# Optimization experiments

Measured on AMD Instinct MI355X. Metric: run time of the kernel, lower is better.

## Reference

```python
import jax, jax.numpy as jnp
import numpy as np

DIM = 64  # QK head dim, matches init kwarg 'dim'

def setup_inputs() -> dict:
    key = jax.random.key(0)
    kq, kk, kv = jax.random.split(key, 3)
    B, L, C, D, H = 2, 2048, 16, DIM, 64
    query = jax.random.normal(kq, (B, L, C, D), dtype=jnp.float32)
    k_ = jax.random.normal(kk, (B, L, C, D), dtype=jnp.float32)
    value = jax.random.normal(kv, (B, L, C, H), dtype=jnp.float32)
    return {"query": query, "key": k_, "value": value}

def reference(query, key, value):
    scaler = 1.0 / jnp.sqrt(jnp.float32(DIM))
    # score: [b, c, l, m]
    score = jnp.einsum('blcd,bmcd->bclm', query, key) * scaler
    # mask=False, dropout=0 -> identity
    attn = jax.nn.softmax(score, axis=3)
    # out: [b, l, c, h]
    out = jnp.einsum('bmch,bclm->blch', value, attn)
    return out
```

## Files before the change

kernel.cpp:

```cpp
#include <hip/hip_runtime.h>
#include <hip/hip_bf16.h>
#include <stdint.h>

#define B_ 2
#define L_ 2048
#define C_ 16
#define D_ 64
#define H_ 64
#define QBLK 128
#define KVBLK 64
#define NTILES 32
#define NTHREADS 256
#define NHEADS 32
#define TILE_ELEMS 4096
#define TENSOR_ELEMS (NHEADS * NTILES * TILE_ELEMS)

typedef __attribute__((ext_vector_type(8))) short bf16x8;
typedef __attribute__((ext_vector_type(16))) float f32x16;
typedef __attribute__((ext_vector_type(8))) unsigned short u16x8;

__device__ inline unsigned short f2bf(float f) {
  union { float f; unsigned int u; } v; v.f = f;
  unsigned int u = v.u;
  unsigned int r = (u + 0x7FFFu + ((u >> 16) & 1u)) >> 16;
  return (unsigned short)r;
}

__device__ inline float fast_exp2(float x) {
#if __has_builtin(__builtin_amdgcn_exp2f)
  return __builtin_amdgcn_exp2f(x);
#else
  return exp2f(x);
#endif
}

__device__ inline unsigned cvt_pk_bf16(float lo, float hi) {
  unsigned r;
  asm("v_cvt_pk_bf16_f32 %0, %1, %2" : "=v"(r) : "v"(lo), "v"(hi));
  return r;
}

__device__ inline void pl32swap(unsigned &x, unsigned &y) {
#if __has_builtin(__builtin_amdgcn_permlane32_swap)
  auto r = __builtin_amdgcn_permlane32_swap(x, y, false, false);
  x = r[0]; y = r[1];
#else
  asm("v_permlane32_swap_b32 %0, %1" : "+v"(x), "+&v"(y));
#endif
}

__device__ inline float xsum32(float v) {
  unsigned x = __float_as_uint(v), y = x;
  pl32swap(x, y);
  return __uint_as_float(x) + __uint_as_float(y);
}

__global__ __launch_bounds__(256) void prepack_kernel(
    const float* __restrict__ Kg, const float* __restrict__ Vg,
    unsigned short* __restrict__ Kb, unsigned short* __restrict__ Vb) {
  int idx = blockIdx.x * 256 + threadIdx.x;
  if (idx < 524288) {
    int i = idx;
    int lane = i & 63, frag = (i >> 6) & 7, t = (i >> 9) & 31, head = i >> 14;
    int b = head >> 4, c = head & 15;
    int ks = frag >> 1, half = frag & 1;
    int row = half * 32 + (lane & 31);
    int kb = ks * 16 + (lane >> 5) * 8;
    const float* src = Kg + ((size_t)(b * L_ + t * 64 + row) * C_ + c) * D_ + kb;
    float4 a0 = ((const float4*)src)[0];
    float4 a1 = ((const float4*)src)[1];
    u16x8 pk;
    pk[0] = f2bf(a0.x); pk[1] = f2bf(a0.y); pk[2] = f2bf(a0.z); pk[3] = f2bf(a0.w);
    pk[4] = f2bf(a1.x); pk[5] = f2bf(a1.y); pk[6] = f2bf(a1.z); pk[7] = f2bf(a1.w);
    size_t dst = ((((size_t)(head * 32 + t)) * 8 + frag) * 64 + lane) * 8;
    *(u16x8*)&Kb[dst] = pk;
  } else {
    int i = idx - 524288;
    int lane = i & 63, frag = (i >> 6) & 7, t = (i >> 9) & 31, head = i >> 14;
    int b = head >> 4, c = head & 15;
    int m = frag >> 1, half = frag & 1;
    int h = half * 32 + (lane & 31);
    int kv0 = m * 16 + (lane >> 5) * 8;
    const float* src = Vg + ((size_t)(b * L_ + t * 64 + kv0) * C_ + c) * H_ + h;
    u16x8 pv;
#pragma unroll
    for (int j = 0; j < 8; ++j) pv[j] = f2bf(src[(size_t)j * C_ * H_]);
    size_t dst = ((((size_t)(head * 32 + t)) * 8 + frag) * 64 + lane) * 8;
    *(u16x8*)&Vb[dst] = pv;
  }
}

#define SM_PV(S0, S1, O0, O1, L)                                                  \
  {                                                                               \
    float rst[4];                                                                 \
    bf16x8 pf[4];                                                                 \
    _Pragma("unroll")                                                             \
    for (int tq = 0; tq < 4; ++tq) {                                              \
      const int be = ((2 * tq) & 3) * 4;                                          \
      const int bo = ((2 * tq + 1) & 3) * 4;                                      \
      float p0[4], p1[4];                                                         \
      _Pragma("unroll")                                                           \
      for (int r = 0; r < 4; ++r) {                                               \
        float se = (tq < 2) ? S0[be + r] : S1[be + r];                            \
        float so_ = (tq < 2) ? S0[bo + r] : S1[bo + r];                           \
        p0[r] = fast_exp2(se);                                                    \
        p1[r] = fast_exp2(so_);                                                   \
      }                                                                           \
      rst[tq] = ((p0[0] + p0[1]) + (p0[2] + p0[3])) +                             \
                ((p1[0] + p1[1]) + (p1[2] + p1[3]));                              \
      unsigned x0 = cvt_pk_bf16(p0[0], p0[1]);                                    \
      unsigned x1 = cvt_pk_bf16(p0[2], p0[3]);                                    \
      unsigned y0 = cvt_pk_bf16(p1[0], p1[1]);                                    \
      unsigned y1 = cvt_pk_bf16(p1[2], p1[3]);                                    \
      pl32swap(x0, y0);                                                           \
      pl32swap(x1, y1);                                                           \
      union { unsigned wd[4]; bf16x8 v; } pk_;                                    \
      pk_.wd[0] = x0; pk_.wd[1] = x1; pk_.wd[2] = y0; pk_.wd[3] = y1;             \
      pf[tq] = pk_.v;                                                             \
    }                                                                             \
    L += (rst[0] + rst[1]) + (rst[2] + rst[3]);                                   \
    __builtin_amdgcn_s_setprio(1);                                                \
    O0 = __builtin_amdgcn_mfma_f32_32x32x16_bf16(vc00, pf[0], O0, 0, 0, 0);       \
    O1 = __builtin_amdgcn_mfma_f32_32x32x16_bf16(vc01, pf[0], O1, 0, 0, 0);       \
    O0 = __builtin_amdgcn_mfma_f32_32x32x16_bf16(vc02, pf[1], O0, 0, 0, 0);       \
    O1 = __builtin_amdgcn_mfma_f32_32x32x16_bf16(vc03, pf[1], O1, 0, 0, 0);       \
    O0 = __builtin_amdgcn_mfma_f32_32x32x16_bf16(vc10, pf[2], O0, 0, 0, 0);       \
    O1 = __builtin_amdgcn_mfma_f32_32x32x16_bf16(vc11, pf[2], O1, 0, 0, 0);       \
    O0 = __builtin_amdgcn_mfma_f32_32x32x16_bf16(vc12, pf[3], O0, 0, 0, 0);       \
    O1 = __builtin_amdgcn_mfma_f32_32x32x16_bf16(vc13, pf[3], O1, 0, 0, 0);       \
    __builtin_amdgcn_s_setprio(0);                                                \
  }

__global__ __launch_bounds__(NTHREADS, 2) void attn_fwd_kernel(
    const float* __restrict__ Qg,
    const unsigned short* __restrict__ Kb,
    const unsigned short* __restrict__ Vb,
    float* __restrict__ Og) {
  __shared__ float Osh[2 * 64 * 68];
  __shared__ float lsh[2 * 2 * 64];

  const int tid  = threadIdx.x;
  const int lane = tid & 63;
  const int w    = tid >> 6;
  const int qw   = w >> 1;
  const int g    = w & 1;
  const int ql   = lane & 31;
  const int u    = lane >> 5;

  const int bid   = blockIdx.x;
  const int swz   = (bid & 7) * 64 + (bid >> 3);
  const int head  = swz >> 4;
  const int qtile = swz & 15;
  const int b     = head >> 4;
  const int c     = head & 15;
  const int q0    = qtile * QBLK + qw * 64;

  const unsigned short* KbL = Kb + (size_t)head * NTILES * TILE_ELEMS + lane * 8;
  const unsigned short* VbL = Vb + (size_t)head * NTILES * TILE_ELEMS + lane * 8;

  const float sc2 = 0.125f * 1.44269504088896340736f;
  bf16x8 qf0[4], qf1[4];
#pragma unroll
  for (int h = 0; h < 2; ++h) {
    const int qr = q0 + h * 32 + ql;
    const float* qrow = Qg + ((size_t)(b * L_ + qr) * C_ + c) * D_;
#pragma unroll
    for (int ks = 0; ks < 4; ++ks) {
      float4 a0 = *(const float4*)(qrow + ks * 16 + u * 8);
      float4 a1 = *(const float4*)(qrow + ks * 16 + u * 8 + 4);
      bf16x8 q8;
      q8[0] = (short)f2bf(a0.x * sc2); q8[1] = (short)f2bf(a0.y * sc2);
      q8[2] = (short)f2bf(a0.z * sc2); q8[3] = (short)f2bf(a0.w * sc2);
      q8[4] = (short)f2bf(a1.x * sc2); q8[5] = (short)f2bf(a1.y * sc2);
      q8[6] = (short)f2bf(a1.z * sc2); q8[7] = (short)f2bf(a1.w * sc2);
      if (h == 0) qf0[ks] = q8; else qf1[ks] = q8;
    }
  }

  f32x16 o00, o01, o10, o11;
#pragma unroll
  for (int i = 0; i < 16; ++i) { o00[i] = 0.f; o01[i] = 0.f; o10[i] = 0.f; o11[i] = 0.f; }
  float l0 = 0.f, l1 = 0.f;

  bf16x8 kc00, kc01, kc02, kc03;
  {
    const unsigned short* K0 = KbL + (size_t)g * TILE_ELEMS;
    kc00 = *(const bf16x8*)(K0);
    kc01 = *(const bf16x8*)(K0 + 512);
    kc02 = *(const bf16x8*)(K0 + 1024);
    kc03 = *(const bf16x8*)(K0 + 1536);
  }

  for (int tt = 0; tt < NTILES / 2; ++tt) {
    const int t = g + 2 * tt;
    const int tn = (tt + 1 < NTILES / 2) ? t + 2 : t;
    const unsigned short* Kt = KbL + (size_t)t * TILE_ELEMS;
    const unsigned short* Vt = VbL + (size_t)t * TILE_ELEMS;

    bf16x8 kc10 = *(const bf16x8*)(Kt + 2048);
    bf16x8 kc11 = *(const bf16x8*)(Kt + 2560);
    bf16x8 kc12 = *(const bf16x8*)(Kt + 3072);
    bf16x8 kc13 = *(const bf16x8*)(Kt + 3584);
    bf16x8 vc00 = *(const bf16x8*)(Vt);
    bf16x8 vc01 = *(const bf16x8*)(Vt + 512);
    bf16x8 vc02 = *(const bf16x8*)(Vt + 1024);
    bf16x8 vc03 = *(const bf16x8*)(Vt + 1536);
    bf16x8 vc10 = *(const bf16x8*)(Vt + 2048);
    bf16x8 vc11 = *(const bf16x8*)(Vt + 2560);
    bf16x8 vc12 = *(const bf16x8*)(Vt + 3072);
    bf16x8 vc13 = *(const bf16x8*)(Vt + 3584);

    f32x16 s00, s01, s10, s11;
#pragma unroll
    for (int i = 0; i < 16; ++i) { s00[i] = 0.f; s01[i] = 0.f; s10[i] = 0.f; s11[i] = 0.f; }
    __builtin_amdgcn_s_setprio(1);
    s00 = __builtin_amdgcn_mfma_f32_32x32x16_bf16(kc00, qf0[0], s00, 0, 0, 0);
    s01 = __builtin_amdgcn_mfma_f32_32x32x16_bf16(kc01, qf0[0], s01, 0, 0, 0);
    s10 = __builtin_amdgcn_mfma_f32_32x32x16_bf16(kc00, qf1[0], s10, 0, 0, 0);
    s11 = __builtin_amdgcn_mfma_f32_32x32x16_bf16(kc01, qf1[0], s11, 0, 0, 0);
    s00 = __builtin_amdgcn_mfma_f32_32x32x16_bf16(kc02, qf0[1], s00, 0, 0, 0);
    s01 = __builtin_amdgcn_mfma_f32_32x32x16_bf16(kc03, qf0[1], s01, 0, 0, 0);
    s10 = __builtin_amdgcn_mfma_f32_32x32x16_bf16(kc02, qf1[1], s10, 0, 0, 0);
    s11 = __builtin_amdgcn_mfma_f32_32x32x16_bf16(kc03, qf1[1], s11, 0, 0, 0);
    s00 = __builtin_amdgcn_mfma_f32_32x32x16_bf16(kc10, qf0[2], s00, 0, 0, 0);
    s01 = __builtin_amdgcn_mfma_f32_32x32x16_bf16(kc11, qf0[2], s01, 0, 0, 0);
    s10 = __builtin_amdgcn_mfma_f32_32x32x16_bf16(kc10, qf1[2], s10, 0, 0, 0);
    s11 = __builtin_amdgcn_mfma_f32_32x32x16_bf16(kc11, qf1[2], s11, 0, 0, 0);
    s00 = __builtin_amdgcn_mfma_f32_32x32x16_bf16(kc12, qf0[3], s00, 0, 0, 0);
    s01 = __builtin_amdgcn_mfma_f32_32x32x16_bf16(kc13, qf0[3], s01, 0, 0, 0);
    s10 = __builtin_amdgcn_mfma_f32_32x32x16_bf16(kc12, qf1[3], s10, 0, 0, 0);
    s11 = __builtin_amdgcn_mfma_f32_32x32x16_bf16(kc13, qf1[3], s11, 0, 0, 0);
    __builtin_amdgcn_s_setprio(0);

    {
      const unsigned short* Kn = KbL + (size_t)tn * TILE_ELEMS;
      kc00 = *(const bf16x8*)(Kn);
      kc01 = *(const bf16x8*)(Kn + 512);
      kc02 = *(const bf16x8*)(Kn + 1024);
      kc03 = *(const bf16x8*)(Kn + 1536);
    }

    SM_PV(s00, s01, o00, o01, l0);
    SM_PV(s10, s11, o10, o11, l1);
  }

  float la0 = xsum32(l0), la1 = xsum32(l1);
  float* Ow = &Osh[(qw * 64 + lane) * 68];
  if (g == 1) {
#pragma unroll
    for (int rg = 0; rg < 4; ++rg) {
      *(float4*)(Ow + rg * 4)      = (float4){o00[rg*4+0], o00[rg*4+1], o00[rg*4+2], o00[rg*4+3]};
      *(float4*)(Ow + 16 + rg * 4) = (float4){o01[rg*4+0], o01[rg*4+1], o01[rg*4+2], o01[rg*4+3]};
      *(float4*)(Ow + 32 + rg * 4) = (float4){o10[rg*4+0], o10[rg*4+1], o10[rg*4+2], o10[rg*4+3]};
      *(float4*)(Ow + 48 + rg * 4) = (float4){o11[rg*4+0], o11[rg*4+1], o11[rg*4+2], o11[rg*4+3]};
    }
    lsh[(qw * 2 + 0) * 64 + lane] = la0;
    lsh[(qw * 2 + 1) * 64 + lane] = la1;
  }
  __syncthreads();
  if (g == 0) {
    const float inv0 = 1.0f / (la0 + lsh[(qw * 2 + 0) * 64 + lane]);
    const float inv1 = 1.0f / (la1 + lsh[(qw * 2 + 1) * 64 + lane]);
    const int qr0 = q0 + ql;
    const int qr1 = q0 + 32 + ql;
    float* orow0 = Og + ((size_t)(b * L_ + qr0) * C_ + c) * H_;
    float* orow1 = Og + ((size_t)(b * L_ + qr1) * C_ + c) * H_;
#pragma unroll
    for (int rg = 0; rg < 4; ++rg) {
      float4 a0 = *(const float4*)(Ow + rg * 4);
      float4 a1 = *(const float4*)(Ow + 16 + rg * 4);
      float4 a2 = *(const float4*)(Ow + 32 + rg * 4);
      float4 a3 = *(const float4*)(Ow + 48 + rg * 4);
      float4 v0, v1, v2, v3;
      v0.x = (o00[rg*4+0] + a0.x) * inv0; v0.y = (o00[rg*4+1] + a0.y) * inv0;
      v0.z = (o00[rg*4+2] + a0.z) * inv0; v0.w = (o00[rg*4+3] + a0.w) * inv0;
      v1.x = (o01[rg*4+0] + a1.x) * inv0; v1.y = (o01[rg*4+1] + a1.y) * inv0;
      v1.z = (o01[rg*4+2] + a1.z) * inv0; v1.w = (o01[rg*4+3] + a1.w) * inv0;
      v2.x = (o10[rg*4+0] + a2.x) * inv1; v2.y = (o10[rg*4+1] + a2.y) * inv1;
      v2.z = (o10[rg*4+2] + a2.z) * inv1; v2.w = (o10[rg*4+3] + a2.w) * inv1;
      v3.x = (o11[rg*4+0] + a3.x) * inv1; v3.y = (o11[rg*4+1] + a3.y) * inv1;
      v3.z = (o11[rg*4+2] + a3.z) * inv1; v3.w = (o11[rg*4+3] + a3.w) * inv1;
      *(float4*)(orow0 + 8 * rg + 4 * u) = v0;
      *(float4*)(orow0 + 32 + 8 * rg + 4 * u) = v1;
      *(float4*)(orow1 + 8 * rg + 4 * u) = v2;
      *(float4*)(orow1 + 32 + 8 * rg + 4 * u) = v3;
    }
  }
}

extern "C" void kernel_launch(void* const* d_in, const int* in_sizes, int n_in,
                              void* d_out, int out_size, void* d_ws, size_t ws_size,
                              hipStream_t stream) {
  const float* Qg = (const float*)d_in[0];
  const float* Kg = (const float*)d_in[1];
  const float* Vg = (const float*)d_in[2];
  float* Og = (float*)d_out;

  unsigned short* Kb = (unsigned short*)d_ws;
  unsigned short* Vb = Kb + (size_t)TENSOR_ELEMS;

  prepack_kernel<<<4096, 256, 0, stream>>>(Kg, Vg, Kb, Vb);

  dim3 grid(NHEADS * (L_ / QBLK));
  dim3 block(NTHREADS);
  attn_fwd_kernel<<<grid, block, 0, stream>>>(Qg, Kb, Vb, Og);
}
```

Before: 64.89 us.

## Rotate K/V fragment registers and merge PV MFMAs across both query halves

Reuses two rotating sets of four bf16x8 register fragments (ka*, kb*) for K and V operands, interleaving their loads between the QK and PV MFMA groups, instead of holding twelve fragments live at once. The softmax for both query halves now runs first, and the PV MFMAs for both halves are then issued together and share each V fragment. The aim is lower register pressure and loads that are software-pipelined behind MFMA work. The trade-off is that more loads now sit directly on the dependency chain between MFMA groups, which can expose load latency.

```diff
diff --git a/kernel.cpp b/kernel.cpp
--- a/kernel.cpp
+++ b/kernel.cpp
@@ -90,10 +90,9 @@
   }
 }
 
-#define SM_PV(S0, S1, O0, O1, L)                                                  \
+#define SM(S0, S1, PF, L)                                                         \
   {                                                                               \
     float rst[4];                                                                 \
-    bf16x8 pf[4];                                                                 \
     _Pragma("unroll")                                                             \
     for (int tq = 0; tq < 4; ++tq) {                                              \
       const int be = ((2 * tq) & 3) * 4;                                          \
@@ -116,19 +115,9 @@
       pl32swap(x1, y1);                                                           \
       union { unsigned wd[4]; bf16x8 v; } pk_;                                    \
       pk_.wd[0] = x0; pk_.wd[1] = x1; pk_.wd[2] = y0; pk_.wd[3] = y1;             \
-      pf[tq] = pk_.v;                                                             \
+      PF[tq] = pk_.v;                                                             \
     }                                                                             \
     L += (rst[0] + rst[1]) + (rst[2] + rst[3]);                                   \
-    __builtin_amdgcn_s_setprio(1);                                                \
-    O0 = __builtin_amdgcn_mfma_f32_32x32x16_bf16(vc00, pf[0], O0, 0, 0, 0);       \
-    O1 = __builtin_amdgcn_mfma_f32_32x32x16_bf16(vc01, pf[0], O1, 0, 0, 0);       \
-    O0 = __builtin_amdgcn_mfma_f32_32x32x16_bf16(vc02, pf[1], O0, 0, 0, 0);       \
-    O1 = __builtin_amdgcn_mfma_f32_32x32x16_bf16(vc03, pf[1], O1, 0, 0, 0);       \
-    O0 = __builtin_amdgcn_mfma_f32_32x32x16_bf16(vc10, pf[2], O0, 0, 0, 0);       \
-    O1 = __builtin_amdgcn_mfma_f32_32x32x16_bf16(vc11, pf[2], O1, 0, 0, 0);       \
-    O0 = __builtin_amdgcn_mfma_f32_32x32x16_bf16(vc12, pf[3], O0, 0, 0, 0);       \
-    O1 = __builtin_amdgcn_mfma_f32_32x32x16_bf16(vc13, pf[3], O1, 0, 0, 0);       \
-    __builtin_amdgcn_s_setprio(0);                                                \
   }
 
 __global__ __launch_bounds__(NTHREADS, 2) void attn_fwd_kernel(
@@ -182,13 +171,13 @@
   for (int i = 0; i < 16; ++i) { o00[i] = 0.f; o01[i] = 0.f; o10[i] = 0.f; o11[i] = 0.f; }
   float l0 = 0.f, l1 = 0.f;
 
-  bf16x8 kc00, kc01, kc02, kc03;
+  bf16x8 ka0, ka1, ka2, ka3;
   {
     const unsigned short* K0 = KbL + (size_t)g * TILE_ELEMS;
-    kc00 = *(const bf16x8*)(K0);
-    kc01 = *(const bf16x8*)(K0 + 512);
-    kc02 = *(const bf16x8*)(K0 + 1024);
-    kc03 = *(const bf16x8*)(K0 + 1536);
+    ka0 = *(const bf16x8*)(K0);
+    ka1 = *(const bf16x8*)(K0 + 512);
+    ka2 = *(const bf16x8*)(K0 + 1024);
+    ka3 = *(const bf16x8*)(K0 + 1536);
   }
 
   for (int tt = 0; tt < NTILES / 2; ++tt) {
@@ -196,52 +185,75 @@
     const int tn = (tt + 1 < NTILES / 2) ? t + 2 : t;
     const unsigned short* Kt = KbL + (size_t)t * TILE_ELEMS;
     const unsigned short* Vt = VbL + (size_t)t * TILE_ELEMS;
-
-    bf16x8 kc10 = *(const bf16x8*)(Kt + 2048);
-    bf16x8 kc11 = *(const bf16x8*)(Kt + 2560);
-    bf16x8 kc12 = *(const bf16x8*)(Kt + 3072);
-    bf16x8 kc13 = *(const bf16x8*)(Kt + 3584);
-    bf16x8 vc00 = *(const bf16x8*)(Vt);
-    bf16x8 vc01 = *(const bf16x8*)(Vt + 512);
-    bf16x8 vc02 = *(const bf16x8*)(Vt + 1024);
-    bf16x8 vc03 = *(const bf16x8*)(Vt + 1536);
-    bf16x8 vc10 = *(const bf16x8*)(Vt + 2048);
-    bf16x8 vc11 = *(const bf16x8*)(Vt + 2560);
-    bf16x8 vc12 = *(const bf16x8*)(Vt + 3072);
-    bf16x8 vc13 = *(const bf16x8*)(Vt + 3584);
+    const unsigned short* Kn = KbL + (size_t)tn * TILE_ELEMS;
 
     f32x16 s00, s01, s10, s11;
 #pragma unroll
     for (int i = 0; i < 16; ++i) { s00[i] = 0.f; s01[i] = 0.f; s10[i] = 0.f; s11[i] = 0.f; }
+
+    bf16x8 kb0 = *(const bf16x8*)(Kt + 2048);
+    bf16x8 kb1 = *(const bf16x8*)(Kt + 2560);
+    bf16x8 kb2 = *(const bf16x8*)(Kt + 3072);
+    bf16x8 kb3 = *(const bf16x8*)(Kt + 3584);
     __builtin_amdgcn_s_setprio(1);
-    s00 = __builtin_amdgcn_mfma_f32_32x32x16_bf16(kc00, qf0[0], s00, 0, 0, 0);
-    s01 = __builtin_amdgcn_mfma_f32_32x32x16_bf16(kc01, qf0[0], s01, 0, 0, 0);
-    s10 = __builtin_amdgcn_mfma_f32_32x32x16_bf16(kc00, qf1[0], s10, 0, 0, 0);
-    s11 = __builtin_amdgcn_mfma_f32_32x32x16_bf16(kc01, qf1[0], s11, 0, 0, 0);
-    s00 = __builtin_amdgcn_mfma_f32_32x32x16_bf16(kc02, qf0[1], s00, 0, 0, 0);
-    s01 = __builtin_amdgcn_mfma_f32_32x32x16_bf16(kc03, qf0[1], s01, 0, 0, 0);
-    s10 = __builtin_amdgcn_mfma_f32_32x32x16_bf16(kc02, qf1[1], s10, 0, 0, 0);
-    s11 = __builtin_amdgcn_mfma_f32_32x32x16_bf16(kc03, qf1[1], s11, 0, 0, 0);
-    s00 = __builtin_amdgcn_mfma_f32_32x32x16_bf16(kc10, qf0[2], s00, 0, 0, 0);
-    s01 = __builtin_amdgcn_mfma_f32_32x32x16_bf16(kc11, qf0[2], s01, 0, 0, 0);
-    s10 = __builtin_amdgcn_mfma_f32_32x32x16_bf16(kc10, qf1[2], s10, 0, 0, 0);
-    s11 = __builtin_amdgcn_mfma_f32_32x32x16_bf16(kc11, qf1[2], s11, 0, 0, 0);
-    s00 = __builtin_amdgcn_mfma_f32_32x32x16_bf16(kc12, qf0[3], s00, 0, 0, 0);
-    s01 = __builtin_amdgcn_mfma_f32_32x32x16_bf16(kc13, qf0[3], s01, 0, 0, 0);
-    s10 = __builtin_amdgcn_mfma_f32_32x32x16_bf16(kc12, qf1[3], s10, 0, 0, 0);
-    s11 = __builtin_amdgcn_mfma_f32_32x32x16_bf16(kc13, qf1[3], s11, 0, 0, 0);
+    s00 = __builtin_amdgcn_mfma_f32_32x32x16_bf16(ka0, qf0[0], s00, 0, 0, 0);
+    s01 = __builtin_amdgcn_mfma_f32_32x32x16_bf16(ka1, qf0[0], s01, 0, 0, 0);
+    s10 = __builtin_amdgcn_mfma_f32_32x32x16_bf16(ka0, qf1[0], s10, 0, 0, 0);
+    s11 = __builtin_amdgcn_mfma_f32_32x32x16_bf16(ka1, qf1[0], s11, 0, 0, 0);
+    s00 = __builtin_amdgcn_mfma_f32_32x32x16_bf16(ka2, qf0[1], s00, 0, 0, 0);
+    s01 = __builtin_amdgcn_mfma_f32_32x32x16_bf16(ka3, qf0[1], s01, 0, 0, 0);
+    s10 = __builtin_amdgcn_mfma_f32_32x32x16_bf16(ka2, qf1[1], s10, 0, 0, 0);
+    s11 = __builtin_amdgcn_mfma_f32_32x32x16_bf16(ka3, qf1[1], s11, 0, 0, 0);
     __builtin_amdgcn_s_setprio(0);
 
-    {
-      const unsigned short* Kn = KbL + (size_t)tn * TILE_ELEMS;
-      kc00 = *(const bf16x8*)(Kn);
-      kc01 = *(const bf16x8*)(Kn + 512);
-      kc02 = *(const bf16x8*)(Kn + 1024);
-      kc03 = *(const bf16x8*)(Kn + 1536);
-    }
-
-    SM_PV(s00, s01, o00, o01, l0);
-    SM_PV(s10, s11, o10, o11, l1);
+    ka0 = *(const bf16x8*)(Vt);
+    ka1 = *(const bf16x8*)(Vt + 512);
+    ka2 = *(const bf16x8*)(Vt + 1024);
+    ka3 = *(const bf16x8*)(Vt + 1536);
+    __builtin_amdgcn_s_setprio(1);
+    s00 = __builtin_amdgcn_mfma_f32_32x32x16_bf16(kb0, qf0[2], s00, 0, 0, 0);
+    s01 = __builtin_amdgcn_mfma_f32_32x32x16_bf16(kb1, qf0[2], s01, 0, 0, 0);
+    s10 = __builtin_amdgcn_mfma_f32_32x32x16_bf16(kb0, qf1[2], s10, 0, 0, 0);
+    s11 = __builtin_amdgcn_mfma_f32_32x32x16_bf16(kb1, qf1[2], s11, 0, 0, 0);
+    s00 = __builtin_amdgcn_mfma_f32_32x32x16_bf16(kb2, qf0[3], s00, 0, 0, 0);
+    s01 = __builtin_amdgcn_mfma_f32_32x32x16_bf16(kb3, qf0[3], s01, 0, 0, 0);
+    s10 = __builtin_amdgcn_mfma_f32_32x32x16_bf16(kb2, qf1[3], s10, 0, 0, 0);
+    s11 = __builtin_amdgcn_mfma_f32_32x32x16_bf16(kb3, qf1[3], s11, 0, 0, 0);
+    __builtin_amdgcn_s_setprio(0);
+
+    kb0 = *(const bf16x8*)(Vt + 2048);
+    kb1 = *(const bf16x8*)(Vt + 2560);
+    kb2 = *(const bf16x8*)(Vt + 3072);
+    kb3 = *(const bf16x8*)(Vt + 3584);
+    bf16x8 pf0[4], pf1[4];
+    SM(s00, s01, pf0, l0);
+    SM(s10, s11, pf1, l1);
+
+    __builtin_amdgcn_s_setprio(1);
+    o00 = __builtin_amdgcn_mfma_f32_32x32x16_bf16(ka0, pf0[0], o00, 0, 0, 0);
+    o01 = __builtin_amdgcn_mfma_f32_32x32x16_bf16(ka1, pf0[0], o01, 0, 0, 0);
+    o10 = __builtin_amdgcn_mfma_f32_32x32x16_bf16(ka0, pf1[0], o10, 0, 0, 0);
+    o11 = __builtin_amdgcn_mfma_f32_32x32x16_bf16(ka1, pf1[0], o11, 0, 0, 0);
+    o00 = __builtin_amdgcn_mfma_f32_32x32x16_bf16(ka2, pf0[1], o00, 0, 0, 0);
+    o01 = __builtin_amdgcn_mfma_f32_32x32x16_bf16(ka3, pf0[1], o01, 0, 0, 0);
+    o10 = __builtin_amdgcn_mfma_f32_32x32x16_bf16(ka2, pf1[1], o10, 0, 0, 0);
+    o11 = __builtin_amdgcn_mfma_f32_32x32x16_bf16(ka3, pf1[1], o11, 0, 0, 0);
+    __builtin_amdgcn_s_setprio(0);
+
+    ka0 = *(const bf16x8*)(Kn);
+    ka1 = *(const bf16x8*)(Kn + 512);
+    ka2 = *(const bf16x8*)(Kn + 1024);
+    ka3 = *(const bf16x8*)(Kn + 1536);
+    __builtin_amdgcn_s_setprio(1);
+    o00 = __builtin_amdgcn_mfma_f32_32x32x16_bf16(kb0, pf0[2], o00, 0, 0, 0);
+    o01 = __builtin_amdgcn_mfma_f32_32x32x16_bf16(kb1, pf0[2], o01, 0, 0, 0);
+    o10 = __builtin_amdgcn_mfma_f32_32x32x16_bf16(kb0, pf1[2], o10, 0, 0, 0);
+    o11 = __builtin_amdgcn_mfma_f32_32x32x16_bf16(kb1, pf1[2], o11, 0, 0, 0);
+    o00 = __builtin_amdgcn_mfma_f32_32x32x16_bf16(kb2, pf0[3], o00, 0, 0, 0);
+    o01 = __builtin_amdgcn_mfma_f32_32x32x16_bf16(kb3, pf0[3], o01, 0, 0, 0);
+    o10 = __builtin_amdgcn_mfma_f32_32x32x16_bf16(kb2, pf1[3], o10, 0, 0, 0);
+    o11 = __builtin_amdgcn_mfma_f32_32x32x16_bf16(kb3, pf1[3], o11, 0, 0, 0);
+    __builtin_amdgcn_s_setprio(0);
   }
 
   float la0 = xsum32(l0), la1 = xsum32(l1);
```

New measurement: 57.87 us. 1.12x faster.
